# Kernel tuning notes

Hardware: AMD Instinct MI355X
Metric: run time of the kernel (lower is better)

Reference implementation:

```python
import jax, jax.numpy as jnp
import numpy as np

DIM = 1024
N_HEAD = 16
HEAD_DIM = DIM // N_HEAD
HIDDEN = 4 * DIM
EPS = 1e-6
NEG = -1e9


def setup_inputs() -> dict:
    key = jax.random.key(0)
    ks = jax.random.split(key, 9)
    B, T = 2, 2048
    x = jax.random.normal(ks[0], (B, T, DIM), dtype=jnp.float32)
    # additive causal mask [T, T]
    mask = jnp.where(jnp.tril(jnp.ones((T, T), dtype=bool)), 0.0, NEG).astype(jnp.float32)
    s = 0.02
    wq = jax.random.normal(ks[1], (DIM, DIM), dtype=jnp.float32) * s
    wk = jax.random.normal(ks[2], (DIM, DIM), dtype=jnp.float32) * s
    wv = jax.random.normal(ks[3], (DIM, DIM), dtype=jnp.float32) * s
    wo = jax.random.normal(ks[4], (DIM, DIM), dtype=jnp.float32) * s
    w1 = jax.random.normal(ks[5], (DIM, HIDDEN), dtype=jnp.float32) * s
    w2 = jax.random.normal(ks[6], (HIDDEN, DIM), dtype=jnp.float32) * s
    g_attn = jnp.ones((DIM,), dtype=jnp.float32)
    g_ffn = jnp.ones((DIM,), dtype=jnp.float32)
    return {"x": x, "mask": mask, "wq": wq, "wk": wk, "wv": wv, "wo": wo,
            "w1": w1, "w2": w2, "g_attn": g_attn, "g_ffn": g_ffn}


def _rmsnorm(x, g):
    norm = jax.lax.rsqrt(jnp.mean(jnp.square(x), axis=-1, keepdims=True) + EPS)
    return (x * norm) * g


def _attention(x, mask, wq, wk, wv, wo):
    B, T, C = x.shape
    # project and split heads: [B, H, T, D]
    q = (x @ wq).reshape(B, T, N_HEAD, HEAD_DIM).transpose(0, 2, 1, 3)
    k = (x @ wk).reshape(B, T, N_HEAD, HEAD_DIM).transpose(0, 2, 1, 3)
    v = (x @ wv).reshape(B, T, N_HEAD, HEAD_DIM).transpose(0, 2, 1, 3)
    attn = jnp.einsum('bhtd,bhsd->bhts', q, k) / np.sqrt(HEAD_DIM).astype(np.float32)
    attn = attn + mask  # broadcast [T,T] over [B,H,T,T]
    p = jax.nn.softmax(attn, axis=-1)
    out = jnp.einsum('bhts,bhsd->bhtd', p, v)
    out = out.transpose(0, 2, 1, 3).reshape(B, T, C)
    return out @ wo


def reference(x, mask, wq, wk, wv, wo, w1, w2, g_attn, g_ffn):
    x = x + _attention(_rmsnorm(x, g_attn), mask, wq, wk, wv, wo)
    h = _rmsnorm(x, g_ffn)
    return x + (jax.nn.silu(h @ w1) @ w2)
```

## Files before the change

### kernel.cpp

```cpp
#include <hip/hip_runtime.h>
#include <hip/hip_bf16.h>
#include <cstdint>
#include <cstddef>

#define DIM    1024
#define NHEAD  16
#define HDIM   64
#define HIDDEN 4096
#define TSEQ   2048
#define TOKENS 4096

typedef __attribute__((ext_vector_type(4))) float  f32x4;
typedef __attribute__((ext_vector_type(8))) short  short8;
typedef __attribute__((ext_vector_type(8))) __bf16 bf16x8;

__device__ __forceinline__ short f2bf(float f) {
    union { float f; uint32_t u; } v; v.f = f;
    uint32_t u = v.u;
    uint32_t r = (u + 0x7fffu + ((u >> 16) & 1u)) >> 16;
    return (short)r;
}

__device__ __forceinline__ f32x4 mfma_bf16(short8 a, short8 b, f32x4 c) {
    return __builtin_amdgcn_mfma_f32_16x16x32_bf16(
        __builtin_bit_cast(bf16x8, a), __builtin_bit_cast(bf16x8, b), c, 0, 0, 0);
}

__device__ __forceinline__ void ldg_lds16(const void* g, void* l) {
    __builtin_amdgcn_global_load_lds(
        (const __attribute__((address_space(1))) void*)g,
        (__attribute__((address_space(3))) void*)l, 16, 0, 0);
}

__global__ __launch_bounds__(256) void transpose_w(
    const float* __restrict__ W, short* __restrict__ Wt, int K, int N)
{
    __shared__ float tile[64][65];
    const int tid = threadIdx.x;
    const int n0 = blockIdx.x * 64, k0 = blockIdx.y * 64;
    for (int i = tid; i < 4096; i += 256) {
        int r = i >> 6, c = i & 63;
        tile[r][c] = W[(size_t)(k0 + r) * N + n0 + c];
    }
    __syncthreads();
    for (int i = tid; i < 4096; i += 256) {
        int r = i >> 6, c = i & 63;
        Wt[(size_t)(n0 + r) * K + k0 + c] = f2bf(tile[c][r]);
    }
}

__global__ __launch_bounds__(256) void transpose_v(
    const short* __restrict__ qkv, short* __restrict__ Vt)
{
    __shared__ short tile[64][72];
    const int tid = threadIdx.x;
    const int s0 = blockIdx.x * 64, bh = blockIdx.y;
    const int b = bh >> 4, h = bh & 15;
    const short* src = qkv + ((size_t)(b * TSEQ + s0)) * 3072 + 2048 + h * 64;
    for (int i = tid; i < 512; i += 256) {
        int r = i >> 3, cg = i & 7;
        *(short8*)&tile[r][cg * 8] = *(const short8*)(src + (size_t)r * 3072 + cg * 8);
    }
    __syncthreads();
    short* dst = Vt + ((size_t)bh * 64) * TSEQ + s0;
    for (int i = tid; i < 512; i += 256) {
        int d = i >> 3, sg = i & 7;
        short8 o;
#pragma unroll
        for (int j = 0; j < 8; ++j) o[j] = tile[sg * 8 + j][d];
        *(short8*)(dst + (size_t)d * TSEQ + sg * 8) = o;
    }
}

__global__ __launch_bounds__(256) void rmsnorm_k(
    const float* __restrict__ x, const float* __restrict__ g, short* __restrict__ out)
{
    const int t = blockIdx.x, tid = threadIdx.x;
    const int wave = tid >> 6, lane = tid & 63;
    const float4 v = ((const float4*)(x + (size_t)t * DIM))[tid];
    float ss = v.x * v.x + v.y * v.y + v.z * v.z + v.w * v.w;
#pragma unroll
    for (int d = 1; d < 64; d <<= 1) ss += __shfl_xor(ss, d, 64);
    __shared__ float red[4];
    if (lane == 0) red[wave] = ss;
    __syncthreads();
    float tot = red[0] + red[1] + red[2] + red[3];
    float rn = rsqrtf(tot * (1.0f / (float)DIM) + 1e-6f);
    const float4 gv = ((const float4*)g)[tid];
    short4 ov = make_short4(f2bf(v.x * rn * gv.x), f2bf(v.y * rn * gv.y),
                            f2bf(v.z * rn * gv.z), f2bf(v.w * rn * gv.w));
    ((short4*)(out + (size_t)t * DIM))[tid] = ov;
}

template <int EPI>
__global__ __launch_bounds__(256) void gemm_bt(
    const short* __restrict__ A, const short* __restrict__ Bt,
    void* __restrict__ Cout, const float* __restrict__ res,
    int M, int N, int K)
{
    __shared__ short As[128 * 32];
    __shared__ short Bs[128 * 32];
    const int tid  = threadIdx.x;
    const int wave = tid >> 6, lane = tid & 63;
    const int lm = lane & 15, quad = lane >> 4;
    const int wm = wave & 1, wn = wave >> 1;
    const int m0 = blockIdx.y * 128, n0 = blockIdx.x * 128;
    const int Ksl = K / gridDim.z;
    const int kbeg = blockIdx.z * Ksl;

    const f32x4 zero = {0.f, 0.f, 0.f, 0.f};
    f32x4 acc[4][4];
#pragma unroll
    for (int i = 0; i < 4; ++i)
#pragma unroll
        for (int j = 0; j < 4; ++j) acc[i][j] = zero;

    const short* Abase = A + (size_t)m0 * K;
    const short* Bbase = Bt + (size_t)n0 * K;
    const int lrow = wave * 32 + (lane >> 2);
    const int lcol = (lane & 3) * 8;

    for (int k0 = kbeg; k0 < kbeg + Ksl; k0 += 32) {
#pragma unroll
        for (int l = 0; l < 2; ++l) {
            ldg_lds16(Abase + (size_t)(lrow + l * 16) * K + k0 + lcol,
                      &As[(wave * 32 + l * 16) * 32]);
            ldg_lds16(Bbase + (size_t)(lrow + l * 16) * K + k0 + lcol,
                      &Bs[(wave * 32 + l * 16) * 32]);
        }
        __syncthreads();
        short8 af[4], bf[4];
#pragma unroll
        for (int mt = 0; mt < 4; ++mt)
            af[mt] = *(const short8*)&As[(wm * 64 + mt * 16 + lm) * 32 + quad * 8];
#pragma unroll
        for (int nt = 0; nt < 4; ++nt)
            bf[nt] = *(const short8*)&Bs[(wn * 64 + nt * 16 + lm) * 32 + quad * 8];
#pragma unroll
        for (int mt = 0; mt < 4; ++mt)
#pragma unroll
            for (int nt = 0; nt < 4; ++nt)
                acc[mt][nt] = mfma_bf16(af[mt], bf[nt], acc[mt][nt]);
        __syncthreads();
    }

#pragma unroll
    for (int mt = 0; mt < 4; ++mt) {
#pragma unroll
        for (int r = 0; r < 4; ++r) {
            const int row = m0 + wm * 64 + mt * 16 + quad * 4 + r;
#pragma unroll
            for (int nt = 0; nt < 4; ++nt) {
                const int col = n0 + wn * 64 + nt * 16 + lm;
                const size_t idx = (size_t)row * N + col;
                const float v = acc[mt][nt][r];
                if constexpr (EPI == 0) {
                    ((short*)Cout)[idx] = f2bf(v);
                } else if constexpr (EPI == 1) {
                    ((float*)Cout)[idx] = res[idx] + v;
                } else if constexpr (EPI == 2) {
                    ((short*)Cout)[idx] = f2bf(v / (1.0f + __expf(-v)));
                } else {
                    ((float*)Cout)[(size_t)blockIdx.z * M * N + idx] = v;
                }
            }
        }
    }
}

__global__ __launch_bounds__(256) void combine_k(
    const float* __restrict__ p, const float* __restrict__ res,
    float* __restrict__ out, int n)
{
    const int i = blockIdx.x * 256 + threadIdx.x;
    if (i * 4 < n) {
        float4 a = ((const float4*)res)[i];
        float4 b = ((const float4*)p)[i];
        float4 c = ((const float4*)(p + n))[i];
        float4 o = make_float4(a.x + b.x + c.x, a.y + b.y + c.y,
                               a.z + b.z + c.z, a.w + b.w + c.w);
        ((float4*)out)[i] = o;
    }
}

#define LP 72
__global__ __launch_bounds__(128) void attn_k(
    const short* __restrict__ qkv, const short* __restrict__ Vt,
    short* __restrict__ out)
{
    __shared__ short Qs[64 * LP];
    __shared__ short Ks[64 * LP];
    __shared__ short Vts[64 * LP];
    __shared__ short Ps[2][32 * LP];

    const int tid = threadIdx.x, wave = tid >> 6, lane = tid & 63;
    const int lm = lane & 15, quad = lane >> 4;
    const int bh = blockIdx.x;
    const int qt = (gridDim.y - 1) - blockIdx.y;
    const int b = bh >> 4, h = bh & 15;
    const int q0 = qt * 64;

    const int rr = tid >> 3, cg = tid & 7;

    const short* qbase = qkv + ((size_t)(b * TSEQ + q0)) * 3072 + h * 64;
#pragma unroll
    for (int j = 0; j < 4; ++j)
        *(short8*)&Qs[(rr + j * 16) * LP + cg * 8] =
            *(const short8*)(qbase + (size_t)(rr + j * 16) * 3072 + cg * 8);

    const short* kb  = qkv + (size_t)b * TSEQ * 3072 + 1024 + h * 64;
    const short* vtb = Vt + (size_t)bh * 64 * TSEQ;

    short8 kr[4], vr[4];
#pragma unroll
    for (int j = 0; j < 4; ++j) {
        kr[j] = *(const short8*)(kb + (size_t)(rr + j * 16) * 3072 + cg * 8);
        vr[j] = *(const short8*)(vtb + (size_t)(rr + j * 16) * TSEQ + cg * 8);
    }

    const f32x4 zero = {0.f, 0.f, 0.f, 0.f};
    f32x4 o_acc[2][4];
#pragma unroll
    for (int mt = 0; mt < 2; ++mt)
#pragma unroll
        for (int t = 0; t < 4; ++t) o_acc[mt][t] = zero;
    float lsum[2][4] = {{0.f, 0.f, 0.f, 0.f}, {0.f, 0.f, 0.f, 0.f}};

    for (int st = 0; st <= qt; ++st) {
        __syncthreads();
#pragma unroll
        for (int j = 0; j < 4; ++j) {
            *(short8*)&Ks[(rr + j * 16) * LP + cg * 8] = kr[j];
            *(short8*)&Vts[(rr + j * 16) * LP + cg * 8] = vr[j];
        }
        __syncthreads();
        if (st < qt) {
            const size_t sn = (size_t)(st + 1) * 64;
#pragma unroll
            for (int j = 0; j < 4; ++j) {
                kr[j] = *(const short8*)(kb + (sn + rr + j * 16) * 3072 + cg * 8);
                vr[j] = *(const short8*)(vtb + (size_t)(rr + j * 16) * TSEQ + sn + cg * 8);
            }
        }

        f32x4 sa[2][4];
#pragma unroll
        for (int mt = 0; mt < 2; ++mt)
#pragma unroll
            for (int nt = 0; nt < 4; ++nt) sa[mt][nt] = zero;
#pragma unroll
        for (int kk = 0; kk < 2; ++kk) {
            short8 aq0 = *(const short8*)&Qs[(wave * 32 + lm) * LP + kk * 32 + quad * 8];
            short8 aq1 = *(const short8*)&Qs[(wave * 32 + 16 + lm) * LP + kk * 32 + quad * 8];
#pragma unroll
            for (int nt = 0; nt < 4; ++nt) {
                short8 bk = *(const short8*)&Ks[(nt * 16 + lm) * LP + kk * 32 + quad * 8];
                sa[0][nt] = mfma_bf16(aq0, bk, sa[0][nt]);
                sa[1][nt] = mfma_bf16(aq1, bk, sa[1][nt]);
            }
        }

        const int s0 = st * 64;
        const bool band = (st == qt);
#pragma unroll
        for (int mt = 0; mt < 2; ++mt) {
            const int qrow = q0 + wave * 32 + mt * 16 + quad * 4;
#pragma unroll
            for (int nt = 0; nt < 4; ++nt) {
                const int col = s0 + nt * 16 + lm;
#pragma unroll
                for (int r = 0; r < 4; ++r) {
                    float p = __expf(0.125f * sa[mt][nt][r]);
                    if (band && col > qrow + r) p = 0.f;
                    lsum[mt][r] += p;
                    Ps[wave][(mt * 16 + quad * 4 + r) * LP + nt * 16 + lm] =
                        (short)(__builtin_bit_cast(uint32_t, p) >> 16);
                }
            }
        }

#pragma unroll
        for (int kk = 0; kk < 2; ++kk) {
            short8 ap0 = *(const short8*)&Ps[wave][lm * LP + kk * 32 + quad * 8];
            short8 ap1 = *(const short8*)&Ps[wave][(16 + lm) * LP + kk * 32 + quad * 8];
#pragma unroll
            for (int t = 0; t < 4; ++t) {
                short8 bv = *(const short8*)&Vts[(t * 16 + lm) * LP + kk * 32 + quad * 8];
                o_acc[0][t] = mfma_bf16(ap0, bv, o_acc[0][t]);
                o_acc[1][t] = mfma_bf16(ap1, bv, o_acc[1][t]);
            }
        }
    }

#pragma unroll
    for (int mt = 0; mt < 2; ++mt)
#pragma unroll
        for (int r = 0; r < 4; ++r) {
            float s = lsum[mt][r];
#pragma unroll
            for (int d = 1; d < 16; d <<= 1) s += __shfl_xor(s, d, 16);
            lsum[mt][r] = s;
        }

#pragma unroll
    for (int mt = 0; mt < 2; ++mt)
#pragma unroll
        for (int r = 0; r < 4; ++r) {
            const float inv = 1.0f / lsum[mt][r];
            const int token = b * TSEQ + q0 + wave * 32 + mt * 16 + quad * 4 + r;
#pragma unroll
            for (int t = 0; t < 4; ++t)
                out[(size_t)token * 1024 + h * 64 + t * 16 + lm] = f2bf(o_acc[mt][t][r] * inv);
        }
}

extern "C" void kernel_launch(void* const* d_in, const int* in_sizes, int n_in,
                              void* d_out, int out_size, void* d_ws, size_t ws_size,
                              hipStream_t stream)
{
    const float* x      = (const float*)d_in[0];
    const float* wq     = (const float*)d_in[2];
    const float* wk     = (const float*)d_in[3];
    const float* wv     = (const float*)d_in[4];
    const float* wo     = (const float*)d_in[5];
    const float* w1     = (const float*)d_in[6];
    const float* w2     = (const float*)d_in[7];
    const float* g_attn = (const float*)d_in[8];
    const float* g_ffn  = (const float*)d_in[9];
    float* out = (float*)d_out;

    char* ws = (char*)d_ws;
    const size_t MB = 1024 * 1024;
    short* Wqkv_t = (short*)(ws + 0);
    short* Wo_t   = (short*)(ws + 6 * MB);
    short* W1_t   = (short*)(ws + 8 * MB);
    short* xn     = (short*)(ws + 16 * MB);
    short* hbuf   = (short*)(ws + 24 * MB);
    short* qkv    = (short*)(ws + 32 * MB);
    short* Vt     = (short*)(ws + 64 * MB);
    float* x2     = (float*)(ws + 64 * MB);
    short* W2_t   = (short*)(ws + 80 * MB);
    float* pbuf   = (float*)(ws + 0);

    dim3 blk(256);

    transpose_w<<<dim3(16, 16), blk, 0, stream>>>(wq, Wqkv_t, 1024, 1024);
    transpose_w<<<dim3(16, 16), blk, 0, stream>>>(wk, Wqkv_t + (size_t)1024 * 1024, 1024, 1024);
    transpose_w<<<dim3(16, 16), blk, 0, stream>>>(wv, Wqkv_t + (size_t)2048 * 1024, 1024, 1024);
    transpose_w<<<dim3(16, 16), blk, 0, stream>>>(wo, Wo_t, 1024, 1024);
    transpose_w<<<dim3(64, 16), blk, 0, stream>>>(w1, W1_t, 1024, 4096);
    transpose_w<<<dim3(16, 64), blk, 0, stream>>>(w2, W2_t, 4096, 1024);

    rmsnorm_k<<<TOKENS, blk, 0, stream>>>(x, g_attn, xn);

    gemm_bt<0><<<dim3(3072 / 128, TOKENS / 128), blk, 0, stream>>>(
        xn, Wqkv_t, qkv, nullptr, TOKENS, 3072, 1024);

    transpose_v<<<dim3(TSEQ / 64, 32), blk, 0, stream>>>(qkv, Vt);

    attn_k<<<dim3(32, TSEQ / 64), dim3(128), 0, stream>>>(qkv, Vt, xn);

    gemm_bt<1><<<dim3(1024 / 128, TOKENS / 128), blk, 0, stream>>>(
        xn, Wo_t, x2, x, TOKENS, 1024, 1024);

    rmsnorm_k<<<TOKENS, blk, 0, stream>>>(x2, g_ffn, hbuf);

    gemm_bt<2><<<dim3(HIDDEN / 128, TOKENS / 128), blk, 0, stream>>>(
        hbuf, W1_t, qkv, nullptr, TOKENS, HIDDEN, 1024);

    gemm_bt<3><<<dim3(1024 / 128, TOKENS / 128, 2), blk, 0, stream>>>(
        qkv, W2_t, pbuf, nullptr, TOKENS, 1024, HIDDEN);

    combine_k<<<dim3(TOKENS * DIM / 4 / 256), blk, 0, stream>>>(
        pbuf, x2, out, TOKENS * DIM);
}
```

Before: 405.8 us.

## Register-prefetch GEMM tiles and split-K the output projection

```diff
diff --git a/kernel.cpp b/kernel.cpp
--- a/kernel.cpp
+++ b/kernel.cpp
@@ -24,12 +24,6 @@
 __device__ __forceinline__ f32x4 mfma_bf16(short8 a, short8 b, f32x4 c) {
     return __builtin_amdgcn_mfma_f32_16x16x32_bf16(
         __builtin_bit_cast(bf16x8, a), __builtin_bit_cast(bf16x8, b), c, 0, 0, 0);
-}
-
-__device__ __forceinline__ void ldg_lds16(const void* g, void* l) {
-    __builtin_amdgcn_global_load_lds(
-        (const __attribute__((address_space(1))) void*)g,
-        (__attribute__((address_space(3))) void*)l, 16, 0, 0);
 }
 
 __global__ __launch_bounds__(256) void transpose_w(
@@ -106,7 +100,7 @@
     const int wm = wave & 1, wn = wave >> 1;
     const int m0 = blockIdx.y * 128, n0 = blockIdx.x * 128;
     const int Ksl = K / gridDim.z;
-    const int kbeg = blockIdx.z * Ksl;
+    const int kbeg = blockIdx.z * Ksl, kend = kbeg + Ksl;
 
     const f32x4 zero = {0.f, 0.f, 0.f, 0.f};
     f32x4 acc[4][4];
@@ -115,20 +109,34 @@
 #pragma unroll
         for (int j = 0; j < 4; ++j) acc[i][j] = zero;
 
-    const short* Abase = A + (size_t)m0 * K;
-    const short* Bbase = Bt + (size_t)n0 * K;
     const int lrow = wave * 32 + (lane >> 2);
     const int lcol = (lane & 3) * 8;
-
-    for (int k0 = kbeg; k0 < kbeg + Ksl; k0 += 32) {
-#pragma unroll
-        for (int l = 0; l < 2; ++l) {
-            ldg_lds16(Abase + (size_t)(lrow + l * 16) * K + k0 + lcol,
-                      &As[(wave * 32 + l * 16) * 32]);
-            ldg_lds16(Bbase + (size_t)(lrow + l * 16) * K + k0 + lcol,
-                      &Bs[(wave * 32 + l * 16) * 32]);
-        }
+    const short* Ap = A + (size_t)(m0 + lrow) * K + kbeg + lcol;
+    const short* Bp = Bt + (size_t)(n0 + lrow) * K + kbeg + lcol;
+    short* Asw = &As[lrow * 32 + lcol];
+    short* Bsw = &Bs[lrow * 32 + lcol];
+
+    short8 ga0, ga1, gb0, gb1;
+    ga0 = *(const short8*)Ap;
+    ga1 = *(const short8*)(Ap + (size_t)16 * K);
+    gb0 = *(const short8*)Bp;
+    gb1 = *(const short8*)(Bp + (size_t)16 * K);
+    Ap += 32; Bp += 32;
+
+    for (int k0 = kbeg; k0 < kend; k0 += 32) {
         __syncthreads();
+        *(short8*)Asw = ga0;
+        *(short8*)(Asw + 16 * 32) = ga1;
+        *(short8*)Bsw = gb0;
+        *(short8*)(Bsw + 16 * 32) = gb1;
+        __syncthreads();
+        if (k0 + 32 < kend) {
+            ga0 = *(const short8*)Ap;
+            ga1 = *(const short8*)(Ap + (size_t)16 * K);
+            gb0 = *(const short8*)Bp;
+            gb1 = *(const short8*)(Bp + (size_t)16 * K);
+            Ap += 32; Bp += 32;
+        }
         short8 af[4], bf[4];
 #pragma unroll
         for (int mt = 0; mt < 4; ++mt)
@@ -141,7 +149,6 @@
 #pragma unroll
             for (int nt = 0; nt < 4; ++nt)
                 acc[mt][nt] = mfma_bf16(af[mt], bf[nt], acc[mt][nt]);
-        __syncthreads();
     }
 
 #pragma unroll
@@ -337,10 +344,11 @@
     short* xn     = (short*)(ws + 16 * MB);
     short* hbuf   = (short*)(ws + 24 * MB);
     short* qkv    = (short*)(ws + 32 * MB);
+    float* pbufO  = (float*)(ws + 32 * MB);
     short* Vt     = (short*)(ws + 64 * MB);
     float* x2     = (float*)(ws + 64 * MB);
     short* W2_t   = (short*)(ws + 80 * MB);
-    float* pbuf   = (float*)(ws + 0);
+    float* pbuf2  = (float*)(ws + 0);
 
     dim3 blk(256);
 
@@ -360,8 +368,10 @@
 
     attn_k<<<dim3(32, TSEQ / 64), dim3(128), 0, stream>>>(qkv, Vt, xn);
 
-    gemm_bt<1><<<dim3(1024 / 128, TOKENS / 128), blk, 0, stream>>>(
-        xn, Wo_t, x2, x, TOKENS, 1024, 1024);
+    gemm_bt<3><<<dim3(1024 / 128, TOKENS / 128, 2), blk, 0, stream>>>(
+        xn, Wo_t, pbufO, nullptr, TOKENS, 1024, 1024);
+    combine_k<<<dim3(TOKENS * DIM / 4 / 256), blk, 0, stream>>>(
+        pbufO, x, x2, TOKENS * DIM);
 
     rmsnorm_k<<<TOKENS, blk, 0, stream>>>(x2, g_ffn, hbuf);
 
@@ -369,8 +379,8 @@
         hbuf, W1_t, qkv, nullptr, TOKENS, HIDDEN, 1024);
 
     gemm_bt<3><<<dim3(1024 / 128, TOKENS / 128, 2), blk, 0, stream>>>(
-        qkv, W2_t, pbuf, nullptr, TOKENS, 1024, HIDDEN);
+        qkv, W2_t, pbuf2, nullptr, TOKENS, 1024, HIDDEN);
 
     combine_k<<<dim3(TOKENS * DIM / 4 / 256), blk, 0, stream>>>(
-        pbuf, x2, out, TOKENS * DIM);
-}
+        pbuf2, x2, out, TOKENS * DIM);
+}
```

Measured after the change: 379.6 us. 6.5% less time.
